# Kernel tuning notes

Hardware: AMD Instinct MI355X
Metric: run time of the kernel (lower is better)

## Reference

```python
import jax, jax.numpy as jnp
import numpy as np
import math

N_HEADS = 16
D_EMBED = 1024
D_CROSS = 768
FF_DIM = 4096
D_HEAD = D_EMBED // N_HEADS
LN_EPS = 1e-5


def layer_norm(h, g, b):
    mu = jnp.mean(h, axis=-1, keepdims=True)
    var = jnp.var(h, axis=-1, keepdims=True)
    return (h - mu) * jax.lax.rsqrt(var + LN_EPS) * g + b


def mha(q, k, v):
    # q: [B,Sq,D], k/v: [B,Skv,D] -> split heads, attend, merge
    B, Sq, _ = q.shape
    Skv = k.shape[1]
    qh = q.reshape(B, Sq, N_HEADS, D_HEAD).transpose(0, 2, 1, 3)
    kh = k.reshape(B, Skv, N_HEADS, D_HEAD).transpose(0, 2, 1, 3)
    vh = v.reshape(B, Skv, N_HEADS, D_HEAD).transpose(0, 2, 1, 3)
    scores = jnp.einsum('bhqd,bhkd->bhqk', qh, kh) / math.sqrt(D_HEAD)
    attn = jax.nn.softmax(scores, axis=-1)
    out = jnp.einsum('bhqk,bhkd->bhqd', attn, vh)
    return out.transpose(0, 2, 1, 3).reshape(B, Sq, D_EMBED)


def setup_inputs() -> dict:
    key = jax.random.key(0)
    ks = jax.random.split(key, 24)
    s = 0.02
    inp = {
        'x': jax.random.normal(ks[0], (4, 1024, D_EMBED), jnp.float32),
        'y': jax.random.normal(ks[1], (4, 77, D_CROSS), jnp.float32),
        # self-attention in_proj (d_embed -> 3*d_embed) and out_proj
        'w_qkv': jax.random.normal(ks[2], (D_EMBED, 3 * D_EMBED), jnp.float32) * s,
        'b_qkv': jnp.zeros((3 * D_EMBED,), jnp.float32),
        'w_so': jax.random.normal(ks[3], (D_EMBED, D_EMBED), jnp.float32) * s,
        'b_so': jnp.zeros((D_EMBED,), jnp.float32),
        # cross-attention projections
        'w_q': jax.random.normal(ks[4], (D_EMBED, D_EMBED), jnp.float32) * s,
        'b_q': jnp.zeros((D_EMBED,), jnp.float32),
        'w_k': jax.random.normal(ks[5], (D_CROSS, D_EMBED), jnp.float32) * s,
        'b_k': jnp.zeros((D_EMBED,), jnp.float32),
        'w_v': jax.random.normal(ks[6], (D_CROSS, D_EMBED), jnp.float32) * s,
        'b_v': jnp.zeros((D_EMBED,), jnp.float32),
        'w_co': jax.random.normal(ks[7], (D_EMBED, D_EMBED), jnp.float32) * s,
        'b_co': jnp.zeros((D_EMBED,), jnp.float32),
        # 3-layer FFN
        'w1': jax.random.normal(ks[8], (D_EMBED, FF_DIM), jnp.float32) * s,
        'b1': jnp.zeros((FF_DIM,), jnp.float32),
        'w2': jax.random.normal(ks[9], (FF_DIM, FF_DIM), jnp.float32) * s,
        'b2': jnp.zeros((FF_DIM,), jnp.float32),
        'w3': jax.random.normal(ks[10], (FF_DIM, D_EMBED), jnp.float32) * s,
        'b3': jnp.zeros((D_EMBED,), jnp.float32),
        # single shared LayerNorm (used 3 times, as in the torch module)
        'ln_g': jnp.ones((D_EMBED,), jnp.float32),
        'ln_b': jnp.zeros((D_EMBED,), jnp.float32),
    }
    return inp


def reference(x, y, w_qkv, b_qkv, w_so, b_so, w_q, b_q, w_k, b_k, w_v, b_v,
              w_co, b_co, w1, b1, w2, b2, w3, b3, ln_g, ln_b):
    # --- self attention (no causal mask) ---
    qkv = x @ w_qkv + b_qkv
    q, k, v = jnp.split(qkv, 3, axis=-1)
    sa = mha(q, k, v) @ w_so + b_so
    x = layer_norm(x + sa, ln_g, ln_b)
    # --- cross attention ---
    qc = x @ w_q + b_q
    kc = y @ w_k + b_k
    vc = y @ w_v + b_v
    ca = mha(qc, kc, vc) @ w_co + b_co
    x = layer_norm(x + ca, ln_g, ln_b)
    # --- 3-layer FFN with ReLU ---
    h = jax.nn.relu(x @ w1 + b1)
    h = jax.nn.relu(h @ w2 + b2)
    ff = h @ w3 + b3
    x = layer_norm(x + ff, ln_g, ln_b)
    return x
```

## Files before the change

### kernel.cpp

```cpp
#include <hip/hip_runtime.h>
#include <hip/hip_bf16.h>
#include <math.h>

typedef short v8s __attribute__((ext_vector_type(8)));
typedef short v4s __attribute__((ext_vector_type(4)));
typedef float v4f __attribute__((ext_vector_type(4)));

__device__ __forceinline__ unsigned short f2bf(float f) {
  union { float f; unsigned u; } a; a.f = f;
  unsigned u = a.u + 0x7fffu + ((a.u >> 16) & 1u);
  return (unsigned short)(u >> 16);
}

__device__ __forceinline__ void gld_lds16(const unsigned short* g, unsigned short* l) {
  __builtin_amdgcn_global_load_lds(
      (const __attribute__((address_space(1))) void*)g,
      (__attribute__((address_space(3))) void*)l,
      16, 0, 0);
}

__global__ void cvt_f32_bf16(const float* __restrict__ in,
                             unsigned short* __restrict__ out, int n4) {
  int i = blockIdx.x * blockDim.x + threadIdx.x;
  if (i >= n4) return;
  float4 v = reinterpret_cast<const float4*>(in)[i];
  ushort4 o;
  o.x = f2bf(v.x); o.y = f2bf(v.y); o.z = f2bf(v.z); o.w = f2bf(v.w);
  reinterpret_cast<ushort4*>(out)[i] = o;
}

__global__ void cvt_transpose(const float* __restrict__ in,
                              unsigned short* __restrict__ out, int K, int N) {
  __shared__ float t[32][33];
  int bx = blockIdx.x, by = blockIdx.y;
  int tx = threadIdx.x, ty = threadIdx.y;
#pragma unroll
  for (int i = 0; i < 4; i++) {
    int k = by * 32 + ty + i * 8;
    t[ty + i * 8][tx] = in[(size_t)k * N + bx * 32 + tx];
  }
  __syncthreads();
#pragma unroll
  for (int i = 0; i < 4; i++) {
    int n = bx * 32 + ty + i * 8;
    out[(size_t)n * K + by * 32 + tx] = f2bf(t[tx][ty + i * 8]);
  }
}

__global__ __launch_bounds__(256)
void transpose_v(const unsigned short* __restrict__ V,
                 unsigned short* __restrict__ Vt,
                 int rowstride, int batch_rows, int Skv, int kvpad) {
  __shared__ __align__(16) unsigned short t[64][80];
  int ch = blockIdx.x, h = blockIdx.y, b = blockIdx.z;
  int tid = threadIdx.x;
  int sr = tid >> 2, sc = (tid & 3) * 16;
  int gr = ch * 64 + sr;
  v8s v0 = {}, v1 = {};
  if (gr < Skv) {
    const unsigned short* p = V + (size_t)(b * batch_rows + gr) * rowstride + h * 64 + sc;
    v0 = *(const v8s*)p; v1 = *(const v8s*)(p + 8);
  }
  *(v8s*)&t[sr][sc]     = v0;
  *(v8s*)&t[sr][sc + 8] = v1;
  __syncthreads();
  int d  = tid >> 2;
  int k0 = (tid & 3) * 16;
  unsigned short* o = Vt + ((size_t)(b * 16 + h) * 64 + d) * kvpad + ch * 64 + k0;
  v8s o0, o1;
#pragma unroll
  for (int e = 0; e < 8; e++) { o0[e] = t[k0 + e][d]; o1[e] = t[k0 + 8 + e][d]; }
  *(v8s*)o       = o0;
  *(v8s*)(o + 8) = o1;
}

template<bool RELU>
__global__ __launch_bounds__(512, 2)
void gemm256(const unsigned short* __restrict__ A,
             const unsigned short* __restrict__ BT,
             const float* __restrict__ bias,
             unsigned short* __restrict__ Cb,
             int M, int N, int K, int lda, int ldb) {
  __shared__ __align__(16) unsigned short lA[2][2][8192];
  __shared__ __align__(16) unsigned short lB[2][2][8192];
  int tid  = threadIdx.x;
  int lane = tid & 63;
  int wave = tid >> 6;
  int wrow = wave >> 2;
  int wcol = wave & 3;
  int quad = lane >> 4;
  int l15  = lane & 15;
  int m0 = blockIdx.y * 256;
  int n0 = blockIdx.x * 256;
  int NT = K >> 6;

  int srow  = wave * 16 + (lane >> 2);
  int scol8 = ((lane & 3) ^ ((lane >> 3) & 3)) << 3;
  const unsigned short* gA = A  + (size_t)(m0 + srow) * lda + scol8;
  const unsigned short* gB = BT + (size_t)(n0 + srow) * ldb + scol8;
  const size_t rowblkA = (size_t)128 * lda;
  const size_t rowblkB = (size_t)128 * ldb;

  auto stageA = [&](int U, int kh) {
    unsigned short* d = &lA[U & 1][kh][wave * 512];
    const unsigned short* s = gA + (size_t)U * 64 + kh * 32;
    gld_lds16(s, d);
    gld_lds16(s + rowblkA, d + 4096);
  };
  auto stageB = [&](int U, int kh) {
    unsigned short* d = &lB[U & 1][kh][wave * 512];
    const unsigned short* s = gB + (size_t)U * 64 + kh * 32;
    gld_lds16(s, d);
    gld_lds16(s + rowblkB, d + 4096);
  };

  int rsw   = (l15 >> 1) & 3;
  int chOff = ((quad ^ rsw) << 3);
  int aBase = (wrow * 128 + l15) * 32 + chOff;
  int bBase = (wcol * 64  + l15) * 32 + chOff;

  const v4f vzero = {0.f, 0.f, 0.f, 0.f};
  v4f acc[8][4];
#pragma unroll
  for (int i = 0; i < 8; i++)
#pragma unroll
    for (int j = 0; j < 4; j++) acc[i][j] = vzero;

  stageB(0, 0); stageA(0, 0); stageA(0, 1); stageB(0, 1);
  if (NT > 1) {
    stageB(1, 0); stageA(1, 0);
    asm volatile("s_waitcnt vmcnt(4)" ::: "memory");
  } else {
    asm volatile("s_waitcnt vmcnt(0)" ::: "memory");
  }
  __builtin_amdgcn_s_barrier();
  __builtin_amdgcn_sched_barrier(0);

  for (int U = 0; U < NT; ++U) {
    int c = U & 1;
    v8s aF[4], bF[4];

#pragma unroll
    for (int n = 0; n < 4; n++) bF[n] = *(const v8s*)&lB[c][0][bBase + n * 512];
#pragma unroll
    for (int m = 0; m < 4; m++) aF[m] = *(const v8s*)&lA[c][0][aBase + m * 512];
    if (U + 1 < NT) stageA(U + 1, 1);
    __builtin_amdgcn_s_barrier();
    __builtin_amdgcn_s_setprio(1);
#pragma unroll
    for (int m = 0; m < 4; m++)
#pragma unroll
      for (int n = 0; n < 4; n++)
        acc[m][n] = __builtin_amdgcn_mfma_f32_16x16x32_bf16(aF[m], bF[n], acc[m][n], 0, 0, 0);
    __builtin_amdgcn_s_setprio(0);
    __builtin_amdgcn_s_barrier();

#pragma unroll
    for (int m = 0; m < 4; m++) aF[m] = *(const v8s*)&lA[c][0][aBase + (4 + m) * 512];
    if (U + 1 < NT) stageB(U + 1, 1);
    __builtin_amdgcn_s_barrier();
    __builtin_amdgcn_s_setprio(1);
#pragma unroll
    for (int m = 0; m < 4; m++)
#pragma unroll
      for (int n = 0; n < 4; n++)
        acc[4 + m][n] = __builtin_amdgcn_mfma_f32_16x16x32_bf16(aF[m], bF[n], acc[4 + m][n], 0, 0, 0);
    __builtin_amdgcn_s_setprio(0);
    __builtin_amdgcn_s_barrier();

#pragma unroll
    for (int n = 0; n < 4; n++) bF[n] = *(const v8s*)&lB[c][1][bBase + n * 512];
#pragma unroll
    for (int m = 0; m < 4; m++) aF[m] = *(const v8s*)&lA[c][1][aBase + m * 512];
    if (U + 2 < NT) stageB(U + 2, 0);
    __builtin_amdgcn_s_barrier();
    __builtin_amdgcn_s_setprio(1);
#pragma unroll
    for (int m = 0; m < 4; m++)
#pragma unroll
      for (int n = 0; n < 4; n++)
        acc[m][n] = __builtin_amdgcn_mfma_f32_16x16x32_bf16(aF[m], bF[n], acc[m][n], 0, 0, 0);
    __builtin_amdgcn_s_setprio(0);
    __builtin_amdgcn_s_barrier();

#pragma unroll
    for (int m = 0; m < 4; m++) aF[m] = *(const v8s*)&lA[c][1][aBase + (4 + m) * 512];
    if (U + 2 < NT) stageA(U + 2, 0);
    __builtin_amdgcn_s_barrier();
    __builtin_amdgcn_s_setprio(1);
#pragma unroll
    for (int m = 0; m < 4; m++)
#pragma unroll
      for (int n = 0; n < 4; n++)
        acc[4 + m][n] = __builtin_amdgcn_mfma_f32_16x16x32_bf16(aF[m], bF[n], acc[4 + m][n], 0, 0, 0);
    __builtin_amdgcn_s_setprio(0);
    if (U + 2 < NT) asm volatile("s_waitcnt vmcnt(4)" ::: "memory");
    else            asm volatile("s_waitcnt vmcnt(0)" ::: "memory");
    __builtin_amdgcn_s_barrier();
    __builtin_amdgcn_sched_barrier(0);
  }

#pragma unroll
  for (int j = 0; j < 4; j++) {
    int col = n0 + wcol * 64 + j * 16 + l15;
    float bv = bias[col];
#pragma unroll
    for (int i = 0; i < 8; i++) {
      int rb = m0 + wrow * 128 + (i >> 2) * 64 + (i & 3) * 16 + quad * 4;
#pragma unroll
      for (int r = 0; r < 4; r++) {
        int row = rb + r;
        if (row < M) {
          float v = acc[i][j][r] + bv;
          if (RELU) v = fmaxf(v, 0.f);
          Cb[(size_t)row * N + col] = f2bf(v);
        }
      }
    }
  }
}

template<bool RELU, bool OUTF, bool OUTB>
__global__ __launch_bounds__(256)
void gemm_bf16(const unsigned short* __restrict__ A,
               const unsigned short* __restrict__ BT,
               const float* __restrict__ bias,
               float* __restrict__ Cf, float* __restrict__ Cf2,
               unsigned short* __restrict__ Cb,
               int M, int N, int Kred, int ld) {
  __shared__ __align__(16) unsigned short lA[128 * 64];
  __shared__ __align__(16) unsigned short lB[128 * 64];
  int tid  = threadIdx.x;
  int lane = tid & 63;
  int wave = tid >> 6;
  int wr = (wave >> 1) * 64;
  int wc = (wave & 1) * 64;
  int quad = lane >> 4;
  int l15  = lane & 15;
  int m0 = blockIdx.y * 128;
  int n0 = blockIdx.x * 128;
  int z  = blockIdx.z;

  const unsigned short* Az = A  + (size_t)z * Kred;
  const unsigned short* Bz = BT + (size_t)z * Kred;
  float* Cfo = z ? Cf2 : Cf;
  const float* biasz = z ? nullptr : bias;

  int srow   = tid >> 3;
  int schunk = (tid & 7) ^ (srow & 7);
  const unsigned short* gA = Az + (size_t)(m0 + srow) * ld + schunk * 8;
  const unsigned short* gB = Bz + (size_t)(n0 + srow) * ld + schunk * 8;
  unsigned short* ldsA = lA + wave * 512;
  unsigned short* ldsB = lB + wave * 512;
  const size_t rowblk = (size_t)32 * ld;

  const v4f vzero = {0.f, 0.f, 0.f, 0.f};
  v4f acc[4][4];
#pragma unroll
  for (int i = 0; i < 4; i++)
#pragma unroll
    for (int j = 0; j < 4; j++) acc[i][j] = vzero;

  for (int k0 = 0; k0 < Kred; k0 += 64) {
#pragma unroll
    for (int i = 0; i < 4; i++) {
      gld_lds16(gA + k0 + i * rowblk, ldsA + i * 2048);
      gld_lds16(gB + k0 + i * rowblk, ldsB + i * 2048);
    }
    __syncthreads();
#pragma unroll
    for (int s = 0; s < 2; s++) {
      v8s aF[4], bF[4];
#pragma unroll
      for (int i = 0; i < 4; i++)
        aF[i] = *(const v8s*)&lA[(wr + i * 16 + l15) * 64 + (((s * 4 + quad) ^ (l15 & 7)) * 8)];
#pragma unroll
      for (int j = 0; j < 4; j++)
        bF[j] = *(const v8s*)&lB[(wc + j * 16 + l15) * 64 + (((s * 4 + quad) ^ (l15 & 7)) * 8)];
#pragma unroll
      for (int i = 0; i < 4; i++)
#pragma unroll
        for (int j = 0; j < 4; j++)
          acc[i][j] = __builtin_amdgcn_mfma_f32_16x16x32_bf16(aF[i], bF[j], acc[i][j], 0, 0, 0);
    }
    __syncthreads();
  }

#pragma unroll
  for (int j = 0; j < 4; j++) {
    int col = n0 + wc + j * 16 + l15;
    float bv = biasz ? biasz[col] : 0.f;
#pragma unroll
    for (int i = 0; i < 4; i++) {
#pragma unroll
      for (int r = 0; r < 4; r++) {
        int row = m0 + wr + i * 16 + quad * 4 + r;
        if (row < M) {
          float v = acc[i][j][r] + bv;
          if (RELU) v = fmaxf(v, 0.f);
          if (OUTF) Cfo[(size_t)row * N + col] = v;
          if (OUTB && !z) Cb[(size_t)row * N + col] = f2bf(v);
        }
      }
    }
  }
}

__global__ __launch_bounds__(256)
void attn_kernel(const unsigned short* __restrict__ Q,
                 const unsigned short* __restrict__ K,
                 const unsigned short* __restrict__ Vt,
                 unsigned short* __restrict__ O,
                 int q_rowstride, int kv_rowstride, int o_rowstride,
                 int q_batch_rows, int kv_batch_rows, int Skv, int kvpad,
                 float scale) {
  __shared__ __align__(16) unsigned short lK[64][72];
  __shared__ __align__(16) unsigned short lV[64][72];
  __shared__ __align__(16) unsigned short lP[4][16][72];
  int tid  = threadIdx.x;
  int lane = tid & 63;
  int wave = tid >> 6;
  int quad = lane >> 4;
  int l15  = lane & 15;
  int qt = blockIdx.x, h = blockIdx.y, b = blockIdx.z;

  const unsigned short* Qb  = Q  + (size_t)b * q_batch_rows * q_rowstride + h * 64;
  const unsigned short* Kb  = K  + (size_t)b * kv_batch_rows * kv_rowstride + h * 64;
  const unsigned short* Vtb = Vt + ((size_t)(b * 16 + h) * 64) * kvpad;

  v8s qf0, qf1;
  {
    const unsigned short* qr = Qb + (size_t)(qt * 64 + wave * 16 + l15) * q_rowstride + quad * 8;
    qf0 = *(const v8s*)(qr);
    qf1 = *(const v8s*)(qr + 32);
  }

  const v4f vzero = {0.f, 0.f, 0.f, 0.f};
  v4f o_acc[4];
#pragma unroll
  for (int t = 0; t < 4; t++) o_acc[t] = vzero;
  float m_r[4], l_r[4];
#pragma unroll
  for (int r = 0; r < 4; r++) { m_r[r] = -1e30f; l_r[r] = 0.f; }

  int sr = tid >> 2;
  int sc = (tid & 3) * 16;

  int nch = (Skv + 63) >> 6;
  for (int ch = 0; ch < nch; ch++) {
    int base = ch * 64;
    int gr = base + sr;
    v8s k0v = {}, k1v = {};
    if (gr < Skv) {
      const unsigned short* kp = Kb + (size_t)gr * kv_rowstride + sc;
      k0v = *(const v8s*)kp;  k1v = *(const v8s*)(kp + 8);
    }
    const unsigned short* vp = Vtb + (size_t)sr * kvpad + base + sc;
    v8s w0 = *(const v8s*)vp;
    v8s w1 = *(const v8s*)(vp + 8);
    __syncthreads();
    *(v8s*)&lK[sr][sc]     = k0v;
    *(v8s*)&lK[sr][sc + 8] = k1v;
    {
      v4s a0 = {w0[0], w0[1], w0[2], w0[3]};
      v4s a1 = {w0[4], w0[5], w0[6], w0[7]};
      v4s a2 = {w1[0], w1[1], w1[2], w1[3]};
      v4s a3 = {w1[4], w1[5], w1[6], w1[7]};
      *(v4s*)&lV[sr][sc]      = a0;
      *(v4s*)&lV[sr][sc + 4]  = a1;
      *(v4s*)&lV[sr][sc + 8]  = a2;
      *(v4s*)&lV[sr][sc + 12] = a3;
    }
    __syncthreads();

    float s[4][4];
#pragma unroll
    for (int t = 0; t < 4; t++) {
      v8s kf0 = *(const v8s*)&lK[t * 16 + l15][quad * 8];
      v8s kf1 = *(const v8s*)&lK[t * 16 + l15][32 + quad * 8];
      v4f sacc = vzero;
      sacc = __builtin_amdgcn_mfma_f32_16x16x32_bf16(qf0, kf0, sacc, 0, 0, 0);
      sacc = __builtin_amdgcn_mfma_f32_16x16x32_bf16(qf1, kf1, sacc, 0, 0, 0);
      int kvpos = base + t * 16 + l15;
      bool ok = kvpos < Skv;
#pragma unroll
      for (int r = 0; r < 4; r++) s[t][r] = ok ? sacc[r] * scale : -1e30f;
    }

#pragma unroll
    for (int r = 0; r < 4; r++) {
      float mx = fmaxf(fmaxf(s[0][r], s[1][r]), fmaxf(s[2][r], s[3][r]));
#pragma unroll
      for (int d = 1; d < 16; d <<= 1) mx = fmaxf(mx, __shfl_xor(mx, d));
      float mnew = fmaxf(m_r[r], mx);
      float alpha = __expf(m_r[r] - mnew);
      float sm = 0.f;
#pragma unroll
      for (int t = 0; t < 4; t++) { s[t][r] = __expf(s[t][r] - mnew); sm += s[t][r]; }
#pragma unroll
      for (int d = 1; d < 16; d <<= 1) sm += __shfl_xor(sm, d);
      l_r[r] = l_r[r] * alpha + sm;
      m_r[r] = mnew;
#pragma unroll
      for (int t = 0; t < 4; t++) o_acc[t][r] *= alpha;
    }

#pragma unroll
    for (int t = 0; t < 4; t++)
#pragma unroll
      for (int r = 0; r < 4; r++)
        lP[wave][quad * 4 + r][t * 16 + l15] = f2bf(s[t][r]);
    v8s pf0 = *(const v8s*)&lP[wave][l15][quad * 8];
    v8s pf1 = *(const v8s*)&lP[wave][l15][32 + quad * 8];
#pragma unroll
    for (int t = 0; t < 4; t++) {
      v8s vf0 = *(const v8s*)&lV[t * 16 + l15][quad * 8];
      v8s vf1 = *(const v8s*)&lV[t * 16 + l15][32 + quad * 8];
      o_acc[t] = __builtin_amdgcn_mfma_f32_16x16x32_bf16(pf0, vf0, o_acc[t], 0, 0, 0);
      o_acc[t] = __builtin_amdgcn_mfma_f32_16x16x32_bf16(pf1, vf1, o_acc[t], 0, 0, 0);
    }
  }

  int orow0 = b * q_batch_rows + qt * 64 + wave * 16;
#pragma unroll
  for (int t = 0; t < 4; t++) {
#pragma unroll
    for (int r = 0; r < 4; r++) {
      float v = o_acc[t][r] / l_r[r];
      O[(size_t)(orow0 + quad * 4 + r) * o_rowstride + h * 64 + t * 16 + l15] = f2bf(v);
    }
  }
}

__global__ __launch_bounds__(256)
void ln_kernel(const float* base, const float* __restrict__ delta,
               const float* __restrict__ delta2,
               const float* __restrict__ g, const float* __restrict__ bb,
               float* outf, unsigned short* __restrict__ outb) {
  __shared__ float red[8];
  int row = blockIdx.x;
  int tid = threadIdx.x;
  float4 vb = ((const float4*)(base  + (size_t)row * 1024))[tid];
  float4 vd = ((const float4*)(delta + (size_t)row * 1024))[tid];
  float v0 = vb.x + vd.x, v1 = vb.y + vd.y, v2 = vb.z + vd.z, v3 = vb.w + vd.w;
  if (delta2) {
    float4 v2d = ((const float4*)(delta2 + (size_t)row * 1024))[tid];
    v0 += v2d.x; v1 += v2d.y; v2 += v2d.z; v3 += v2d.w;
  }
  float s = v0 + v1 + v2 + v3;
  float q = v0 * v0 + v1 * v1 + v2 * v2 + v3 * v3;
#pragma unroll
  for (int d = 1; d < 64; d <<= 1) { s += __shfl_xor(s, d); q += __shfl_xor(q, d); }
  int wave = tid >> 6, lane = tid & 63;
  if (lane == 0) { red[wave] = s; red[4 + wave] = q; }
  __syncthreads();
  s = red[0] + red[1] + red[2] + red[3];
  q = red[4] + red[5] + red[6] + red[7];
  float mean = s * (1.f / 1024.f);
  float var  = q * (1.f / 1024.f) - mean * mean;
  float rstd = rsqrtf(var + 1e-5f);
  float4 gg  = ((const float4*)g)[tid];
  float4 bv  = ((const float4*)bb)[tid];
  float o0 = (v0 - mean) * rstd * gg.x + bv.x;
  float o1 = (v1 - mean) * rstd * gg.y + bv.y;
  float o2 = (v2 - mean) * rstd * gg.z + bv.z;
  float o3 = (v3 - mean) * rstd * gg.w + bv.w;
  if (outf) {
    float4 o; o.x = o0; o.y = o1; o.z = o2; o.w = o3;
    ((float4*)(outf + (size_t)row * 1024))[tid] = o;
  }
  if (outb) {
    ushort4 u; u.x = f2bf(o0); u.y = f2bf(o1); u.z = f2bf(o2); u.w = f2bf(o3);
    ((ushort4*)(outb + (size_t)row * 1024))[tid] = u;
  }
}

extern "C" void kernel_launch(void* const* d_in, const int* in_sizes, int n_in,
                              void* d_out, int out_size, void* d_ws, size_t ws_size,
                              hipStream_t stream) {
  const float* x     = (const float*)d_in[0];
  const float* y     = (const float*)d_in[1];
  const float* w_qkv = (const float*)d_in[2];
  const float* b_qkv = (const float*)d_in[3];
  const float* w_so  = (const float*)d_in[4];
  const float* b_so  = (const float*)d_in[5];
  const float* w_q   = (const float*)d_in[6];
  const float* b_q   = (const float*)d_in[7];
  const float* w_k   = (const float*)d_in[8];
  const float* b_k   = (const float*)d_in[9];
  const float* w_v   = (const float*)d_in[10];
  const float* b_v   = (const float*)d_in[11];
  const float* w_co  = (const float*)d_in[12];
  const float* b_co  = (const float*)d_in[13];
  const float* w1    = (const float*)d_in[14];
  const float* b1    = (const float*)d_in[15];
  const float* w2    = (const float*)d_in[16];
  const float* b2    = (const float*)d_in[17];
  const float* w3    = (const float*)d_in[18];
  const float* b3    = (const float*)d_in[19];
  const float* ln_g  = (const float*)d_in[20];
  const float* ln_b  = (const float*)d_in[21];

  char* ws = (char*)d_ws;
  auto US = [&](size_t off) { return (unsigned short*)(ws + off); };
  auto FP = [&](size_t off) { return (float*)(ws + off); };

  constexpr size_t o_wqkv = 0;
  constexpr size_t o_wso  = o_wqkv + 3072ull * 1024 * 2;
  constexpr size_t o_wq   = o_wso  + 1024ull * 1024 * 2;
  constexpr size_t o_wk   = o_wq   + 1024ull * 1024 * 2;
  constexpr size_t o_wv   = o_wk   + 1024ull * 768 * 2;
  constexpr size_t o_wco  = o_wv   + 1024ull * 768 * 2;
  constexpr size_t o_w1   = o_wco  + 1024ull * 1024 * 2;
  constexpr size_t o_w2   = o_w1   + 4096ull * 1024 * 2;
  constexpr size_t o_w3   = o_w2   + 4096ull * 4096 * 2;
  constexpr size_t o_xf   = o_w3   + 1024ull * 4096 * 2;
  constexpr size_t o_xbf  = o_xf   + 4096ull * 1024 * 4;
  constexpr size_t o_ybf  = o_xbf  + 4096ull * 1024 * 2;
  constexpr size_t o_dlt  = o_ybf  + 308ull * 768 * 2;
  constexpr size_t o_R1   = o_dlt  + 4096ull * 1024 * 4;
  constexpr size_t o_attn = o_R1   + 4096ull * 3072 * 2;
  constexpr size_t o_R2   = o_attn + 4096ull * 1024 * 2;
  constexpr size_t o_qc  = o_R1;
  constexpr size_t o_kc  = o_R1 + 4096ull * 1024 * 2;
  constexpr size_t o_vc  = o_kc + 308ull * 1024 * 2;
  constexpr size_t o_h1  = o_R1;
  constexpr size_t o_h2  = o_R2;
  constexpr size_t o_dlt2 = o_R1;
  constexpr size_t o_vtS = o_R2;
  constexpr size_t o_vtC = o_R2 + 4ull * 16 * 64 * 1024 * 2;

  dim3 tb(32, 8);
  cvt_transpose<<<dim3(96, 32),  tb, 0, stream>>>(w_qkv, US(o_wqkv), 1024, 3072);
  cvt_transpose<<<dim3(32, 32),  tb, 0, stream>>>(w_so,  US(o_wso),  1024, 1024);
  cvt_transpose<<<dim3(32, 32),  tb, 0, stream>>>(w_q,   US(o_wq),   1024, 1024);
  cvt_transpose<<<dim3(32, 24),  tb, 0, stream>>>(w_k,   US(o_wk),   768,  1024);
  cvt_transpose<<<dim3(32, 24),  tb, 0, stream>>>(w_v,   US(o_wv),   768,  1024);
  cvt_transpose<<<dim3(32, 32),  tb, 0, stream>>>(w_co,  US(o_wco),  1024, 1024);
  cvt_transpose<<<dim3(128, 32), tb, 0, stream>>>(w1,    US(o_w1),   1024, 4096);
  cvt_transpose<<<dim3(128, 128),tb, 0, stream>>>(w2,    US(o_w2),   4096, 4096);
  cvt_transpose<<<dim3(32, 128), tb, 0, stream>>>(w3,    US(o_w3),   4096, 1024);

  cvt_f32_bf16<<<4096, 256, 0, stream>>>(x, US(o_xbf), 4096 * 1024 / 4);
  cvt_f32_bf16<<<231, 256, 0, stream>>>(y, US(o_ybf), 4 * 77 * 768 / 4);

  gemm256<false><<<dim3(12, 16), 512, 0, stream>>>(
      US(o_xbf), US(o_wqkv), b_qkv, US(o_R1), 4096, 3072, 1024, 1024, 1024);
  transpose_v<<<dim3(16, 16, 4), 256, 0, stream>>>(
      US(o_R1) + 2048, US(o_vtS), 3072, 1024, 1024, 1024);
  attn_kernel<<<dim3(16, 16, 4), 256, 0, stream>>>(
      US(o_R1), US(o_R1) + 1024, US(o_vtS), US(o_attn),
      3072, 3072, 1024, 1024, 1024, 1024, 1024, 0.125f);
  gemm_bf16<false, true, false><<<dim3(8, 32, 2), 256, 0, stream>>>(
      US(o_attn), US(o_wso), b_so, FP(o_dlt), FP(o_dlt2), nullptr, 4096, 1024, 512, 1024);
  ln_kernel<<<4096, 256, 0, stream>>>(x, FP(o_dlt), FP(o_dlt2), ln_g, ln_b,
                                      FP(o_xf), US(o_xbf));

  gemm_bf16<false, false, true><<<dim3(8, 32, 1), 256, 0, stream>>>(
      US(o_xbf), US(o_wq), b_q, nullptr, nullptr, US(o_qc), 4096, 1024, 1024, 1024);
  gemm_bf16<false, false, true><<<dim3(8, 3, 1), 256, 0, stream>>>(
      US(o_ybf), US(o_wk), b_k, nullptr, nullptr, US(o_kc), 308, 1024, 768, 768);
  gemm_bf16<false, false, true><<<dim3(8, 3, 1), 256, 0, stream>>>(
      US(o_ybf), US(o_wv), b_v, nullptr, nullptr, US(o_vc), 308, 1024, 768, 768);
  transpose_v<<<dim3(2, 16, 4), 256, 0, stream>>>(
      US(o_vc), US(o_vtC), 1024, 77, 77, 128);
  attn_kernel<<<dim3(16, 16, 4), 256, 0, stream>>>(
      US(o_qc), US(o_kc), US(o_vtC), US(o_attn),
      1024, 1024, 1024, 1024, 77, 77, 128, 0.125f);
  gemm_bf16<false, true, false><<<dim3(8, 32, 2), 256, 0, stream>>>(
      US(o_attn), US(o_wco), b_co, FP(o_dlt), FP(o_dlt2), nullptr, 4096, 1024, 512, 1024);
  ln_kernel<<<4096, 256, 0, stream>>>(FP(o_xf), FP(o_dlt), FP(o_dlt2), ln_g, ln_b,
                                      FP(o_xf), US(o_xbf));

  gemm256<true><<<dim3(16, 16), 512, 0, stream>>>(
      US(o_xbf), US(o_w1), b1, US(o_h1), 4096, 4096, 1024, 1024, 1024);
  gemm256<true><<<dim3(16, 16), 512, 0, stream>>>(
      US(o_h1), US(o_w2), b2, US(o_h2), 4096, 4096, 4096, 4096, 4096);
  gemm_bf16<false, true, false><<<dim3(8, 32, 2), 256, 0, stream>>>(
      US(o_h2), US(o_w3), b3, FP(o_dlt), FP(o_dlt2), nullptr, 4096, 1024, 2048, 4096);
  ln_kernel<<<4096, 256, 0, stream>>>(FP(o_xf), FP(o_dlt), FP(o_dlt2), ln_g, ln_b,
                                      (float*)d_out, nullptr);
}
```

Measured before the change: 755.8 us.

## Software-pipeline LDS fragment loads one phase ahead of MFMA in GEMM mainloop

Result: no change. 757.7 us (+0.3%).

```diff
diff --git a/kernel.cpp b/kernel.cpp
--- a/kernel.cpp
+++ b/kernel.cpp
@@ -18,6 +18,8 @@
       (__attribute__((address_space(3))) void*)l,
       16, 0, 0);
 }
+
+#define VMCNT(n) asm volatile("s_waitcnt vmcnt(" #n ")" ::: "memory")
 
 __global__ void cvt_f32_bf16(const float* __restrict__ in,
                              unsigned short* __restrict__ out, int n4) {
@@ -126,26 +128,26 @@
 #pragma unroll
     for (int j = 0; j < 4; j++) acc[i][j] = vzero;
 
-  stageB(0, 0); stageA(0, 0); stageA(0, 1); stageB(0, 1);
-  if (NT > 1) {
-    stageB(1, 0); stageA(1, 0);
-    asm volatile("s_waitcnt vmcnt(4)" ::: "memory");
-  } else {
-    asm volatile("s_waitcnt vmcnt(0)" ::: "memory");
-  }
+  stageB(0, 0); stageA(0, 0);
+  stageB(0, 1); stageA(0, 1);
+  if (NT > 1) { stageB(1, 0); stageA(1, 0); VMCNT(8); }
+  else        { VMCNT(4); }
   __builtin_amdgcn_s_barrier();
-  __builtin_amdgcn_sched_barrier(0);
+
+  v8s aF[4], aF2[4], bF[4], bF2[4];
+#pragma unroll
+  for (int n = 0; n < 4; n++) bF[n] = *(const v8s*)&lB[0][0][bBase + n * 512];
+#pragma unroll
+  for (int m = 0; m < 4; m++) aF[m] = *(const v8s*)&lA[0][0][aBase + m * 512];
 
   for (int U = 0; U < NT; ++U) {
-    int c = U & 1;
-    v8s aF[4], bF[4];
-
-#pragma unroll
-    for (int n = 0; n < 4; n++) bF[n] = *(const v8s*)&lB[c][0][bBase + n * 512];
-#pragma unroll
-    for (int m = 0; m < 4; m++) aF[m] = *(const v8s*)&lA[c][0][aBase + m * 512];
-    if (U + 1 < NT) stageA(U + 1, 1);
+    int c  = U & 1;
+    int cn = c ^ 1;
+
+    if (U + 1 < NT) stageB(U + 1, 1);
     __builtin_amdgcn_s_barrier();
+#pragma unroll
+    for (int m = 0; m < 4; m++) aF2[m] = *(const v8s*)&lA[c][0][aBase + (4 + m) * 512];
     __builtin_amdgcn_s_setprio(1);
 #pragma unroll
     for (int m = 0; m < 4; m++)
@@ -153,51 +155,52 @@
       for (int n = 0; n < 4; n++)
         acc[m][n] = __builtin_amdgcn_mfma_f32_16x16x32_bf16(aF[m], bF[n], acc[m][n], 0, 0, 0);
     __builtin_amdgcn_s_setprio(0);
+
+    if (U + 1 < NT) { VMCNT(6); stageA(U + 1, 1); }
+    else            { VMCNT(0); }
     __builtin_amdgcn_s_barrier();
-
-#pragma unroll
-    for (int m = 0; m < 4; m++) aF[m] = *(const v8s*)&lA[c][0][aBase + (4 + m) * 512];
-    if (U + 1 < NT) stageB(U + 1, 1);
-    __builtin_amdgcn_s_barrier();
+#pragma unroll
+    for (int n = 0; n < 4; n++) bF2[n] = *(const v8s*)&lB[c][1][bBase + n * 512];
+#pragma unroll
+    for (int m = 0; m < 4; m++) aF[m]  = *(const v8s*)&lA[c][1][aBase + m * 512];
     __builtin_amdgcn_s_setprio(1);
 #pragma unroll
     for (int m = 0; m < 4; m++)
 #pragma unroll
       for (int n = 0; n < 4; n++)
-        acc[4 + m][n] = __builtin_amdgcn_mfma_f32_16x16x32_bf16(aF[m], bF[n], acc[4 + m][n], 0, 0, 0);
+        acc[4 + m][n] = __builtin_amdgcn_mfma_f32_16x16x32_bf16(aF2[m], bF[n], acc[4 + m][n], 0, 0, 0);
     __builtin_amdgcn_s_setprio(0);
-    __builtin_amdgcn_s_barrier();
-
-#pragma unroll
-    for (int n = 0; n < 4; n++) bF[n] = *(const v8s*)&lB[c][1][bBase + n * 512];
-#pragma unroll
-    for (int m = 0; m < 4; m++) aF[m] = *(const v8s*)&lA[c][1][aBase + m * 512];
+
     if (U + 2 < NT) stageB(U + 2, 0);
     __builtin_amdgcn_s_barrier();
+#pragma unroll
+    for (int m = 0; m < 4; m++) aF2[m] = *(const v8s*)&lA[c][1][aBase + (4 + m) * 512];
     __builtin_amdgcn_s_setprio(1);
 #pragma unroll
     for (int m = 0; m < 4; m++)
 #pragma unroll
       for (int n = 0; n < 4; n++)
-        acc[m][n] = __builtin_amdgcn_mfma_f32_16x16x32_bf16(aF[m], bF[n], acc[m][n], 0, 0, 0);
+        acc[m][n] = __builtin_amdgcn_mfma_f32_16x16x32_bf16(aF[m], bF2[n], acc[m][n], 0, 0, 0);
     __builtin_amdgcn_s_setprio(0);
-    __builtin_amdgcn_s_barrier();
-
-#pragma unroll
-    for (int m = 0; m < 4; m++) aF[m] = *(const v8s*)&lA[c][1][aBase + (4 + m) * 512];
+
+    if (U + 1 < NT) {
+      if (U + 2 < NT) VMCNT(6); else VMCNT(4);
+    }
     if (U + 2 < NT) stageA(U + 2, 0);
     __builtin_amdgcn_s_barrier();
+    if (U + 1 < NT) {
+#pragma unroll
+      for (int n = 0; n < 4; n++) bF[n] = *(const v8s*)&lB[cn][0][bBase + n * 512];
+#pragma unroll
+      for (int m = 0; m < 4; m++) aF[m] = *(const v8s*)&lA[cn][0][aBase + m * 512];
+    }
     __builtin_amdgcn_s_setprio(1);
 #pragma unroll
     for (int m = 0; m < 4; m++)
 #pragma unroll
       for (int n = 0; n < 4; n++)
-        acc[4 + m][n] = __builtin_amdgcn_mfma_f32_16x16x32_bf16(aF[m], bF[n], acc[4 + m][n], 0, 0, 0);
+        acc[4 + m][n] = __builtin_amdgcn_mfma_f32_16x16x32_bf16(aF2[m], bF2[n], acc[4 + m][n], 0, 0, 0);
     __builtin_amdgcn_s_setprio(0);
-    if (U + 2 < NT) asm volatile("s_waitcnt vmcnt(4)" ::: "memory");
-    else            asm volatile("s_waitcnt vmcnt(0)" ::: "memory");
-    __builtin_amdgcn_s_barrier();
-    __builtin_amdgcn_sched_barrier(0);
   }
 
 #pragma unroll
```

## Restructure 256x256 GEMM LDS layout and pipeline to keep A fragments resident

Applied to the files above, without the earlier changes.

Measured after the change: 754.3 us. Within noise of the previous version (-0.2%).

```diff
diff --git a/kernel.cpp b/kernel.cpp
--- a/kernel.cpp
+++ b/kernel.cpp
@@ -18,6 +18,9 @@
       (__attribute__((address_space(3))) void*)l,
       16, 0, 0);
 }
+
+#define VMCNT(n)  asm volatile("s_waitcnt vmcnt(" #n ")" ::: "memory")
+#define LGKM(n)   asm volatile("s_waitcnt lgkmcnt(" #n ")" ::: "memory")
 
 __global__ void cvt_f32_bf16(const float* __restrict__ in,
                              unsigned short* __restrict__ out, int n4) {
@@ -73,6 +76,18 @@
   *(v8s*)o       = o0;
   *(v8s*)(o + 8) = o1;
 }
+
+#define PH_MFMA(AFR, IB, JB)                                                   \
+  _Pragma("unroll")                                                            \
+  for (int m = 0; m < 4; m++) {                                                \
+    _Pragma("unroll")                                                          \
+    for (int n = 0; n < 2; n++) {                                              \
+      acc[IB + m][JB + n] = __builtin_amdgcn_mfma_f32_16x16x32_bf16(           \
+          AFR[m][0], bF[n][0], acc[IB + m][JB + n], 0, 0, 0);                  \
+      acc[IB + m][JB + n] = __builtin_amdgcn_mfma_f32_16x16x32_bf16(           \
+          AFR[m][1], bF[n][1], acc[IB + m][JB + n], 0, 0, 0);                  \
+    }                                                                          \
+  }
 
 template<bool RELU>
 __global__ __launch_bounds__(512, 2)
@@ -94,30 +109,25 @@
   int n0 = blockIdx.x * 256;
   int NT = K >> 6;
 
-  int srow  = wave * 16 + (lane >> 2);
-  int scol8 = ((lane & 3) ^ ((lane >> 3) & 3)) << 3;
-  const unsigned short* gA = A  + (size_t)(m0 + srow) * lda + scol8;
-  const unsigned short* gB = BT + (size_t)(n0 + srow) * ldb + scol8;
-  const size_t rowblkA = (size_t)128 * lda;
-  const size_t rowblkB = (size_t)128 * ldb;
-
-  auto stageA = [&](int U, int kh) {
-    unsigned short* d = &lA[U & 1][kh][wave * 512];
-    const unsigned short* s = gA + (size_t)U * 64 + kh * 32;
-    gld_lds16(s, d);
-    gld_lds16(s + rowblkA, d + 4096);
+  int lrow = lane >> 3;
+  int swz8 = ((lane & 7) ^ lrow) << 3;
+  const unsigned short* gA0 = A + (size_t)(m0 + wave * 8 + lrow) * lda + swz8;
+  int rr = wave * 8 + lrow;
+  int nbase = (rr >> 5) * 64 + (rr & 31);
+  const unsigned short* gB0 = BT + (size_t)(n0 + nbase) * ldb + swz8;
+
+  auto stageA = [&](int U, int h, int rlo) {
+    unsigned short* d = &lA[U & 1][h][(rlo + wave * 8) * 64];
+    gld_lds16(gA0 + (size_t)(h * 128 + rlo) * lda + (size_t)U * 64, d);
   };
-  auto stageB = [&](int U, int kh) {
-    unsigned short* d = &lB[U & 1][kh][wave * 512];
-    const unsigned short* s = gB + (size_t)U * 64 + kh * 32;
-    gld_lds16(s, d);
-    gld_lds16(s + rowblkB, d + 4096);
+  auto stageB = [&](int U, int hB, int q) {
+    unsigned short* d = &lB[U & 1][hB][(q * 64 + wave * 8) * 64];
+    gld_lds16(gB0 + (size_t)(q * 128 + hB * 32) * ldb + (size_t)U * 64, d);
   };
 
-  int rsw   = (l15 >> 1) & 3;
-  int chOff = ((quad ^ rsw) << 3);
-  int aBase = (wrow * 128 + l15) * 32 + chOff;
-  int bBase = (wcol * 64  + l15) * 32 + chOff;
+  int ch0 = (quad ^ (l15 & 7)) << 3;
+  int ch1 = ch0 ^ 32;
+  int wcol32 = wcol * 32;
 
   const v4f vzero = {0.f, 0.f, 0.f, 0.f};
   v4f acc[8][4];
@@ -126,83 +136,94 @@
 #pragma unroll
     for (int j = 0; j < 4; j++) acc[i][j] = vzero;
 
-  stageB(0, 0); stageA(0, 0); stageA(0, 1); stageB(0, 1);
+  v8s aF0[4][2], aF1[4][2], bF[2][2];
+
+  stageA(0, 0, 0);  stageA(0, 1, 0);
+  stageB(0, 0, 0);  stageB(0, 0, 1);
+  stageA(0, 0, 64); stageA(0, 1, 64);
+  stageB(0, 1, 0);  stageB(0, 1, 1);
   if (NT > 1) {
-    stageB(1, 0); stageA(1, 0);
-    asm volatile("s_waitcnt vmcnt(4)" ::: "memory");
+    stageA(1, 0, 0);  stageA(1, 1, 0);
+    stageB(1, 0, 0);  stageB(1, 0, 1);
+    stageA(1, 0, 64); stageA(1, 1, 64);
+    VMCNT(8);
   } else {
-    asm volatile("s_waitcnt vmcnt(0)" ::: "memory");
+    VMCNT(0);
   }
   __builtin_amdgcn_s_barrier();
-  __builtin_amdgcn_sched_barrier(0);
 
   for (int U = 0; U < NT; ++U) {
     int c = U & 1;
-    v8s aF[4], bF[4];
-
-#pragma unroll
-    for (int n = 0; n < 4; n++) bF[n] = *(const v8s*)&lB[c][0][bBase + n * 512];
-#pragma unroll
-    for (int m = 0; m < 4; m++) aF[m] = *(const v8s*)&lA[c][0][aBase + m * 512];
-    if (U + 1 < NT) stageA(U + 1, 1);
-    __builtin_amdgcn_s_barrier();
+    bool tail = (U + 3 >= NT);
+    const unsigned short* pA  = &lA[c][wrow][0];
+    const unsigned short* pB0 = &lB[c][0][0];
+    const unsigned short* pB1 = &lB[c][1][0];
+
+#pragma unroll
+    for (int m = 0; m < 4; m++) {
+      int ro = (m * 16 + l15) * 64;
+      aF0[m][0] = *(const v8s*)&pA[ro + ch0];
+      aF0[m][1] = *(const v8s*)&pA[ro + ch1];
+    }
+#pragma unroll
+    for (int n = 0; n < 2; n++) {
+      int ro = (wcol32 + n * 16 + l15) * 64;
+      bF[n][0] = *(const v8s*)&pB0[ro + ch0];
+      bF[n][1] = *(const v8s*)&pB0[ro + ch1];
+    }
+    if (U + 1 < NT) { stageB(U + 1, 1, 0); stageB(U + 1, 1, 1); }
+    LGKM(8);
+    __builtin_amdgcn_s_barrier();
+    LGKM(0);
+    __builtin_amdgcn_sched_barrier(0);
     __builtin_amdgcn_s_setprio(1);
-#pragma unroll
-    for (int m = 0; m < 4; m++)
-#pragma unroll
-      for (int n = 0; n < 4; n++)
-        acc[m][n] = __builtin_amdgcn_mfma_f32_16x16x32_bf16(aF[m], bF[n], acc[m][n], 0, 0, 0);
+    PH_MFMA(aF0, 0, 0)
     __builtin_amdgcn_s_setprio(0);
     __builtin_amdgcn_s_barrier();
 
 #pragma unroll
-    for (int m = 0; m < 4; m++) aF[m] = *(const v8s*)&lA[c][0][aBase + (4 + m) * 512];
-    if (U + 1 < NT) stageB(U + 1, 1);
-    __builtin_amdgcn_s_barrier();
+    for (int m = 0; m < 4; m++) {
+      int ro = (64 * 64) + (m * 16 + l15) * 64;
+      aF1[m][0] = *(const v8s*)&pA[ro + ch0];
+      aF1[m][1] = *(const v8s*)&pA[ro + ch1];
+    }
+    if (U + 2 < NT) { stageA(U + 2, 0, 0); stageA(U + 2, 1, 0); }
+    __builtin_amdgcn_s_barrier();
+    LGKM(0);
+    __builtin_amdgcn_sched_barrier(0);
     __builtin_amdgcn_s_setprio(1);
-#pragma unroll
-    for (int m = 0; m < 4; m++)
-#pragma unroll
-      for (int n = 0; n < 4; n++)
-        acc[4 + m][n] = __builtin_amdgcn_mfma_f32_16x16x32_bf16(aF[m], bF[n], acc[4 + m][n], 0, 0, 0);
+    PH_MFMA(aF1, 4, 0)
     __builtin_amdgcn_s_setprio(0);
-    __builtin_amdgcn_s_barrier();
-
-#pragma unroll
-    for (int n = 0; n < 4; n++) bF[n] = *(const v8s*)&lB[c][1][bBase + n * 512];
-#pragma unroll
-    for (int m = 0; m < 4; m++) aF[m] = *(const v8s*)&lA[c][1][aBase + m * 512];
-    if (U + 2 < NT) stageB(U + 2, 0);
-    __builtin_amdgcn_s_barrier();
+    if (tail) { VMCNT(0); } else { VMCNT(10); }
+    __builtin_amdgcn_s_barrier();
+
+#pragma unroll
+    for (int n = 0; n < 2; n++) {
+      int ro = (wcol32 + n * 16 + l15) * 64;
+      bF[n][0] = *(const v8s*)&pB1[ro + ch0];
+      bF[n][1] = *(const v8s*)&pB1[ro + ch1];
+    }
+    if (U + 2 < NT) { stageB(U + 2, 0, 0); stageB(U + 2, 0, 1); }
+    __builtin_amdgcn_s_barrier();
+    LGKM(0);
+    __builtin_amdgcn_sched_barrier(0);
     __builtin_amdgcn_s_setprio(1);
-#pragma unroll
-    for (int m = 0; m < 4; m++)
-#pragma unroll
-      for (int n = 0; n < 4; n++)
-        acc[m][n] = __builtin_amdgcn_mfma_f32_16x16x32_bf16(aF[m], bF[n], acc[m][n], 0, 0, 0);
+    PH_MFMA(aF1, 4, 2)
     __builtin_amdgcn_s_setprio(0);
     __builtin_amdgcn_s_barrier();
 
-#pragma unroll
-    for (int m = 0; m < 4; m++) aF[m] = *(const v8s*)&lA[c][1][aBase + (4 + m) * 512];
-    if (U + 2 < NT) stageA(U + 2, 0);
+    if (U + 2 < NT) { stageA(U + 2, 0, 64); stageA(U + 2, 1, 64); }
     __builtin_amdgcn_s_barrier();
     __builtin_amdgcn_s_setprio(1);
-#pragma unroll
-    for (int m = 0; m < 4; m++)
-#pragma unroll
-      for (int n = 0; n < 4; n++)
-        acc[4 + m][n] = __builtin_amdgcn_mfma_f32_16x16x32_bf16(aF[m], bF[n], acc[4 + m][n], 0, 0, 0);
+    PH_MFMA(aF0, 0, 2)
     __builtin_amdgcn_s_setprio(0);
-    if (U + 2 < NT) asm volatile("s_waitcnt vmcnt(4)" ::: "memory");
-    else            asm volatile("s_waitcnt vmcnt(0)" ::: "memory");
-    __builtin_amdgcn_s_barrier();
-    __builtin_amdgcn_sched_barrier(0);
+    if (tail) { VMCNT(0); } else { VMCNT(8); }
+    __builtin_amdgcn_s_barrier();
   }
 
 #pragma unroll
   for (int j = 0; j < 4; j++) {
-    int col = n0 + wcol * 64 + j * 16 + l15;
+    int col = n0 + wcol * 64 + (j >> 1) * 32 + (j & 1) * 16 + l15;
     float bv = bias[col];
 #pragma unroll
     for (int i = 0; i < 8; i++) {
```
